# Kernel tuning notes

Hardware: AMD Instinct MI355X
Metric: run time of the kernel (lower is better)

The kernel has to match this reference:

```python
import jax, jax.numpy as jnp
import numpy as np

LN_EPS = 1e-5


def _gru_scan(xg, w_hh, b_hh, H, reverse):
    # xg: [T, B, 3H] precomputed input-gate activations (W_ih x + b_ih)
    B = xg.shape[1]
    h0 = jnp.zeros((B, H), xg.dtype)

    def step(h, xt):
        hg = h @ w_hh.T + b_hh                      # [B, 3H]
        r = jax.nn.sigmoid(xt[:, :H] + hg[:, :H])
        z = jax.nn.sigmoid(xt[:, H:2 * H] + hg[:, H:2 * H])
        n = jnp.tanh(xt[:, 2 * H:] + r * hg[:, 2 * H:])
        h = (1.0 - z) * n + z * h
        return h, h

    _, ys = jax.lax.scan(step, h0, xg, reverse=reverse)
    return ys                                       # [T, B, H]


def setup_inputs() -> dict:
    key = jax.random.key(0)
    ks = jax.random.split(key, 12)
    B, T, I, H = 32, 1000, 512, 512
    s = 1.0 / np.sqrt(H)
    u = lambda k, shape: jax.random.uniform(k, shape, jnp.float32, -s, s)
    return {
        "x": jax.random.normal(ks[0], (B, T, I), jnp.float32),
        "ln_gamma": jnp.ones((I,), jnp.float32),
        "ln_beta": jnp.zeros((I,), jnp.float32),
        "w_ih_f": u(ks[1], (3 * H, I)),
        "w_hh_f": u(ks[2], (3 * H, H)),
        "b_ih_f": u(ks[3], (3 * H,)),
        "b_hh_f": u(ks[4], (3 * H,)),
        "w_ih_b": u(ks[5], (3 * H, I)),
        "w_hh_b": u(ks[6], (3 * H, H)),
        "b_ih_b": u(ks[7], (3 * H,)),
        "b_hh_b": u(ks[8], (3 * H,)),
    }


def reference(x, ln_gamma, ln_beta, w_ih_f, w_hh_f, b_ih_f, b_hh_f,
              w_ih_b, w_hh_b, b_ih_b, b_hh_b):
    H = w_hh_f.shape[1]
    # LayerNorm over last dim
    mu = jnp.mean(x, axis=-1, keepdims=True)
    var = jnp.var(x, axis=-1, keepdims=True)
    xn = (x - mu) * jax.lax.rsqrt(var + LN_EPS) * ln_gamma + ln_beta
    # ReLU6
    xn = jnp.clip(xn, 0.0, 6.0)
    # batch_first -> time-major [T, B, I]
    xt = jnp.transpose(xn, (1, 0, 2))
    # Precompute input projections for both directions
    xg_f = xt @ w_ih_f.T + b_ih_f                   # [T, B, 3H]
    xg_b = xt @ w_ih_b.T + b_ih_b
    yf = _gru_scan(xg_f, w_hh_f, b_hh_f, H, reverse=False)
    yb = _gru_scan(xg_b, w_hh_b, b_hh_b, H, reverse=True)
    y = jnp.concatenate([yf, yb], axis=-1)          # [T, B, 2H]
    # dropout treated as identity (deterministic reference)
    return jnp.transpose(y, (1, 0, 2))              # [B, T, 2H]
```

## Files before the change

kernel.cpp:

```cpp
#include <hip/hip_runtime.h>


typedef _Float16 half8   __attribute__((ext_vector_type(8)));
typedef _Float16 half2_  __attribute__((ext_vector_type(2)));
typedef float    floatx4 __attribute__((ext_vector_type(4)));
typedef float    floatx2 __attribute__((ext_vector_type(2)));
typedef unsigned int uintx4 __attribute__((ext_vector_type(4)));

#define T_LEN 1000
#define NB    32
#define DIM   512

#define XN_OFF   0
#define HB_OFF   32768000
#define CTR_OFF  32899072
#define WS_NEED  32899328

__device__ __forceinline__ float bf2f(unsigned short b) {
  unsigned int u = ((unsigned int)b) << 16; float f; __builtin_memcpy(&f, &u, 4); return f;
}
__device__ __forceinline__ unsigned short f2bf(float f) {
  unsigned int u; __builtin_memcpy(&u, &f, 4);
  u = (u + 0x7FFFu + ((u >> 16) & 1u)) >> 16;
  return (unsigned short)u;
}

__global__ void init_kernel(unsigned int* ws32) {
  const int base = HB_OFF / 4;
  const int n    = (WS_NEED - HB_OFF) / 4;
  for (int i = blockIdx.x * blockDim.x + threadIdx.x; i < n; i += gridDim.x * blockDim.x)
    ws32[base + i] = 0u;
}

__global__ __launch_bounds__(256) void ln_kernel(const void* __restrict__ xin,
                                                 const void* __restrict__ gam,
                                                 const void* __restrict__ bet,
                                                 unsigned short* __restrict__ xn) {
  const bool bf = (((const unsigned int*)gam)[0] != 0x3F800000u);
  const int w = threadIdx.x >> 6, l = threadIdx.x & 63;
  const int row = blockIdx.x * 4 + w;
  const int b = row / T_LEN, t = row - b * T_LEN;

  float v[8], g[8], be[8];
  if (bf) {
    const unsigned int* xp = (const unsigned int*)xin + (row * 512 + l * 8) / 2;
    uintx4 r4 = *(const uintx4*)xp;
    uintx4 g4 = *(const uintx4*)((const unsigned int*)gam + l * 4);
    uintx4 b4 = *(const uintx4*)((const unsigned int*)bet + l * 4);
#pragma unroll
    for (int j = 0; j < 4; ++j) {
      v[2*j]   = bf2f((unsigned short)(r4[j] & 0xFFFFu));
      v[2*j+1] = bf2f((unsigned short)(r4[j] >> 16));
      g[2*j]   = bf2f((unsigned short)(g4[j] & 0xFFFFu));
      g[2*j+1] = bf2f((unsigned short)(g4[j] >> 16));
      be[2*j]  = bf2f((unsigned short)(b4[j] & 0xFFFFu));
      be[2*j+1] = bf2f((unsigned short)(b4[j] >> 16));
    }
  } else {
    const float* xp = (const float*)xin + (size_t)row * 512 + l * 8;
    floatx4 a0 = *(const floatx4*)xp;
    floatx4 a1 = *(const floatx4*)(xp + 4);
    const float* gp = (const float*)gam + l * 8;
    const float* bp = (const float*)bet + l * 8;
#pragma unroll
    for (int j = 0; j < 4; ++j) {
      v[j] = a0[j]; v[4+j] = a1[j];
      g[j] = gp[j]; g[4+j] = gp[4+j];
      be[j] = bp[j]; be[4+j] = bp[4+j];
    }
  }

  float s1 = 0.f, s2 = 0.f;
#pragma unroll
  for (int j = 0; j < 8; ++j) { s1 += v[j]; s2 += v[j] * v[j]; }
#pragma unroll
  for (int m = 1; m < 64; m <<= 1) { s1 += __shfl_xor(s1, m); s2 += __shfl_xor(s2, m); }
  const float mean = s1 * (1.f / 512.f);
  const float var  = s2 * (1.f / 512.f) - mean * mean;
  const float rstd = rsqrtf(var + 1e-5f);

  unsigned int out[4];
#pragma unroll
  for (int j = 0; j < 4; ++j) {
    float f0 = (v[2*j]   - mean) * rstd * g[2*j]   + be[2*j];
    float f1 = (v[2*j+1] - mean) * rstd * g[2*j+1] + be[2*j+1];
    f0 = fminf(fmaxf(f0, 0.f), 6.f);
    f1 = fminf(fmaxf(f1, 0.f), 6.f);
    half2_ hp = { (_Float16)f0, (_Float16)f1 };
    __builtin_memcpy(&out[j], &hp, 4);
  }
  *(uintx4*)(xn + ((size_t)(t * 32 + b) * 512 + l * 8)) = *(uintx4*)out;
}

#define SMEM_BYTES 125312

__global__ __launch_bounds__(256, 1) void gru_kernel(
    const void* __restrict__ wihF, const void* __restrict__ whhF,
    const void* __restrict__ bihF, const void* __restrict__ bhhF,
    const void* __restrict__ wihB, const void* __restrict__ whhB,
    const void* __restrict__ bihB, const void* __restrict__ bhhB,
    const void* __restrict__ gam,
    const unsigned short* __restrict__ xn,
    unsigned short* __restrict__ hb,
    unsigned int* __restrict__ ctr,
    void* __restrict__ yout) {
  extern __shared__ char smem[];
  _Float16* wih = (_Float16*)smem;
  _Float16* whh = (_Float16*)(smem + 49152);
  float* part = (float*)(smem + 98304);
  float* hown = (float*)(smem + 122880);
  float* bihs = (float*)(smem + 124928);
  float* bhhs = (float*)(smem + 125120);

  const bool bf = (((const unsigned int*)gam)[0] != 0x3F800000u);
  const int tid = threadIdx.x;
  const int w = tid >> 6, l = tid & 63, quad = l >> 4, lan = l & 15;
  const int dir = blockIdx.x >> 5, wg = blockIdx.x & 31, c0 = wg * 16;

  const void* Wg[2] = { dir ? wihB : wihF, dir ? whhB : whhF };
  const void* Bg[2] = { dir ? bihB : bihF, dir ? bhhB : bhhF };

  for (int idx = tid; idx < 6144; idx += 256) {
    const int mat = idx / 3072;
    const int r = idx - mat * 3072;
    const int nt = r >> 10, s = (r >> 6) & 15, ln = r & 63;
    const int row = nt * 512 + c0 + (ln & 15);
    const int k0 = s * 32 + (ln >> 4) * 8;
    float tmp[8];
    if (bf) {
      const unsigned int* p = (const unsigned int*)Wg[mat] + (row * 512 + k0) / 2;
      uintx4 r4 = *(const uintx4*)p;
#pragma unroll
      for (int j = 0; j < 4; ++j) {
        tmp[2*j]   = bf2f((unsigned short)(r4[j] & 0xFFFFu));
        tmp[2*j+1] = bf2f((unsigned short)(r4[j] >> 16));
      }
    } else {
      const float* p = (const float*)Wg[mat] + (size_t)row * 512 + k0;
      floatx4 a0 = *(const floatx4*)p;
      floatx4 a1 = *(const floatx4*)(p + 4);
#pragma unroll
      for (int j = 0; j < 4; ++j) { tmp[j] = a0[j]; tmp[4+j] = a1[j]; }
    }
    _Float16* dst = (mat ? whh : wih) + ((size_t)((nt * 16 + s) * 64 + ln)) * 8;
#pragma unroll
    for (int j = 0; j < 8; ++j) dst[j] = (_Float16)tmp[j];
  }
  if (tid < 96) {
    const int mat = tid / 48, i = tid % 48, g_ = i >> 4, c = i & 15;
    const int gi = g_ * 512 + c0 + c;
    float v = bf ? bf2f(((const unsigned short*)Bg[mat])[gi]) : ((const float*)Bg[mat])[gi];
    (mat ? bhhs : bihs)[i] = v;
  }
  for (int i = tid; i < 512; i += 256) hown[i] = 0.f;
  __syncthreads();

  unsigned int* myctr = ctr + dir * 16;
  const int kh = w & 1;
  unsigned short* hb_d = hb + dir * 2 * 16384;
  const _Float16* wb = (w < 2) ? wih : whh;

  for (int t = 0; t < T_LEN; ++t) {
    const int tt = dir ? (T_LEN - 1 - t) : t;
    const int cur = t & 1, nxt = cur ^ 1;

    floatx4 acc[2][3];
#pragma unroll
    for (int mt = 0; mt < 2; ++mt)
#pragma unroll
      for (int nt = 0; nt < 3; ++nt) acc[mt][nt] = (floatx4){0.f, 0.f, 0.f, 0.f};

    if (w < 2) {
      const _Float16* A = (const _Float16*)xn + (size_t)tt * 16384;
      half8 av[2][8];
#pragma unroll
      for (int si = 0; si < 8; ++si) {
        const int s = kh * 8 + si, k0 = s * 32 + quad * 8;
        av[0][si] = *(const half8*)(A + (lan * 512 + k0));
        av[1][si] = *(const half8*)(A + ((16 + lan) * 512 + k0));
      }
#pragma unroll
      for (int si = 0; si < 8; ++si) {
        const int s = kh * 8 + si;
#pragma unroll
        for (int nt = 0; nt < 3; ++nt) {
          half8 bfr = *(const half8*)(wb + ((size_t)((nt * 16 + s) * 64 + l)) * 8);
          acc[0][nt] = __builtin_amdgcn_mfma_f32_16x16x32_f16(av[0][si], bfr, acc[0][nt], 0, 0, 0);
          acc[1][nt] = __builtin_amdgcn_mfma_f32_16x16x32_f16(av[1][si], bfr, acc[1][nt], 0, 0, 0);
        }
      }
    } else {
      const unsigned long long* A = (const unsigned long long*)(hb_d + cur * 16384);
      union HU { unsigned long long q[2]; half8 h; };
      HU u[2][8];
#pragma unroll
      for (int si = 0; si < 8; ++si) {
        const int s = kh * 8 + si, k0 = s * 32 + quad * 8;
        const unsigned long long* p0 = A + (lan * 512 + k0) / 4;
        const unsigned long long* p1 = A + ((16 + lan) * 512 + k0) / 4;
        u[0][si].q[0] = __hip_atomic_load(p0,     __ATOMIC_RELAXED, __HIP_MEMORY_SCOPE_AGENT);
        u[0][si].q[1] = __hip_atomic_load(p0 + 1, __ATOMIC_RELAXED, __HIP_MEMORY_SCOPE_AGENT);
        u[1][si].q[0] = __hip_atomic_load(p1,     __ATOMIC_RELAXED, __HIP_MEMORY_SCOPE_AGENT);
        u[1][si].q[1] = __hip_atomic_load(p1 + 1, __ATOMIC_RELAXED, __HIP_MEMORY_SCOPE_AGENT);
      }
#pragma unroll
      for (int si = 0; si < 8; ++si) {
        const int s = kh * 8 + si;
#pragma unroll
        for (int nt = 0; nt < 3; ++nt) {
          half8 bfr = *(const half8*)(wb + ((size_t)((nt * 16 + s) * 64 + l)) * 8);
          acc[0][nt] = __builtin_amdgcn_mfma_f32_16x16x32_f16(u[0][si].h, bfr, acc[0][nt], 0, 0, 0);
          acc[1][nt] = __builtin_amdgcn_mfma_f32_16x16x32_f16(u[1][si].h, bfr, acc[1][nt], 0, 0, 0);
        }
      }
    }

#pragma unroll
    for (int mt = 0; mt < 2; ++mt)
#pragma unroll
      for (int nt = 0; nt < 3; ++nt) {
        float* p = part + ((w * 6 + mt * 3 + nt) << 8);
#pragma unroll
        for (int r = 0; r < 4; ++r) p[(quad * 4 + r) * 16 + lan] = acc[mt][nt][r];
      }
    __syncthreads();

    {
      const int b = tid >> 3, cp = tid & 7;
      const int mt = b >> 4, mr = b & 15;
      float hv[2];
#pragma unroll
      for (int e = 0; e < 2; ++e) {
        const int c = cp * 2 + e;
        const int o = mr * 16 + c;
#define PT(W_, NT_) part[(((W_) * 6 + mt * 3 + (NT_)) << 8) + o]
        const float xr = PT(0, 0) + PT(1, 0) + bihs[c];
        const float xz = PT(0, 1) + PT(1, 1) + bihs[16 + c];
        const float xg = PT(0, 2) + PT(1, 2) + bihs[32 + c];
        const float hr = PT(2, 0) + PT(3, 0) + bhhs[c];
        const float hz = PT(2, 1) + PT(3, 1) + bhhs[16 + c];
        const float hg = PT(2, 2) + PT(3, 2) + bhhs[32 + c];
#undef PT
        const float rr = 1.f / (1.f + __expf(-(xr + hr)));
        const float zz = 1.f / (1.f + __expf(-(xz + hz)));
        float a = xg + rr * hg;
        a = fminf(fmaxf(a, -15.f), 15.f);
        const float e2 = __expf(2.f * a);
        const float nn = (e2 - 1.f) / (e2 + 1.f);
        const float hp = hown[b * 16 + c];
        const float hvv = (1.f - zz) * nn + zz * hp;
        hown[b * 16 + c] = hvv;
        hv[e] = hvv;
      }
      half2_ pk = { (_Float16)hv[0], (_Float16)hv[1] };
      unsigned int pu; __builtin_memcpy(&pu, &pk, 4);
      unsigned int* hdst = (unsigned int*)(hb_d + nxt * 16384 + b * 512 + c0 + cp * 2);
      __hip_atomic_store(hdst, pu, __ATOMIC_RELAXED, __HIP_MEMORY_SCOPE_AGENT);
      const size_t yo = ((size_t)b * T_LEN + tt) * 1024 + dir * 512 + c0 + cp * 2;
      if (bf) {
        unsigned int yp = (unsigned int)f2bf(hv[0]) | ((unsigned int)f2bf(hv[1]) << 16);
        *(unsigned int*)((unsigned short*)yout + yo) = yp;
      } else {
        *(floatx2*)((float*)yout + yo) = (floatx2){hv[0], hv[1]};
      }
    }

    if (t < T_LEN - 1) {
      __syncthreads();
      if (tid == 0) {
        __hip_atomic_fetch_add(myctr, 1u, __ATOMIC_RELAXED, __HIP_MEMORY_SCOPE_AGENT);
        const unsigned int tgt = 32u * (unsigned int)(t + 1);
        while (__hip_atomic_load(myctr, __ATOMIC_RELAXED, __HIP_MEMORY_SCOPE_AGENT) < tgt)
          __builtin_amdgcn_s_sleep(1);
      }
      __syncthreads();
    }
  }
}

extern "C" void kernel_launch(void* const* d_in, const int* in_sizes, int n_in,
                              void* d_out, int out_size, void* d_ws, size_t ws_size,
                              hipStream_t stream) {
  if (ws_size < (size_t)WS_NEED) return;

  (void)hipFuncSetAttribute((const void*)gru_kernel,
                            hipFuncAttributeMaxDynamicSharedMemorySize, 131072);

  const void* x   = d_in[0];
  const void* gam = d_in[1];
  const void* bet = d_in[2];
  const void* wihF = d_in[3]; const void* whhF = d_in[4];
  const void* bihF = d_in[5]; const void* bhhF = d_in[6];
  const void* wihB = d_in[7]; const void* whhB = d_in[8];
  const void* bihB = d_in[9]; const void* bhhB = d_in[10];

  unsigned short* xnp = (unsigned short*)((char*)d_ws + XN_OFF);
  unsigned short* hbp = (unsigned short*)((char*)d_ws + HB_OFF);
  unsigned int*   cp  = (unsigned int*)((char*)d_ws + CTR_OFF);

  init_kernel<<<64, 256, 0, stream>>>((unsigned int*)d_ws);
  ln_kernel<<<8000, 256, 0, stream>>>(x, gam, bet, xnp);
  gru_kernel<<<64, 256, SMEM_BYTES, stream>>>(wihF, whhF, bihF, bhhF,
                                              wihB, whhB, bihB, bhhB,
                                              gam, xnp, hbp, cp, d_out);
}
```

Measured before the change: 5.283 ms.

## Overlap next-step input projection with grid barrier wait using per-block flags

Takes the input-projection MFMA for step t+1 off the recurrent critical path. Each block now computes it, together with the prefetch of the following x slice, while it waits for the other blocks to publish h. All four waves now split the K dimension of both matmuls and accumulate into double-buffered LDS partials with atomicAdd. The single shared atomic counter is replaced by per-block flags, polled by 32 threads. This shortens each serial step, at the cost of LDS atomics, extra zeroing passes and more registers.

```diff
diff --git a/kernel.cpp b/kernel.cpp
--- a/kernel.cpp
+++ b/kernel.cpp
@@ -8,13 +8,19 @@
 typedef unsigned int uintx4 __attribute__((ext_vector_type(4)));
 
 #define T_LEN 1000
-#define NB    32
-#define DIM   512
 
 #define XN_OFF   0
 #define HB_OFF   32768000
 #define CTR_OFF  32899072
-#define WS_NEED  32899328
+#define WS_NEED  32903168
+
+#define L_WIH    0
+#define L_WHH    49152
+#define L_PART   98304
+#define L_HOWN   116736
+#define L_BIH    118784
+#define L_BHH    118976
+#define SMEM_BYTES 119168
 
 __device__ __forceinline__ float bf2f(unsigned short b) {
   unsigned int u = ((unsigned int)b) << 16; float f; __builtin_memcpy(&f, &u, 4); return f;
@@ -92,8 +98,6 @@
   *(uintx4*)(xn + ((size_t)(t * 32 + b) * 512 + l * 8)) = *(uintx4*)out;
 }
 
-#define SMEM_BYTES 125312
-
 __global__ __launch_bounds__(256, 1) void gru_kernel(
     const void* __restrict__ wihF, const void* __restrict__ whhF,
     const void* __restrict__ bihF, const void* __restrict__ bhhF,
@@ -102,20 +106,21 @@
     const void* __restrict__ gam,
     const unsigned short* __restrict__ xn,
     unsigned short* __restrict__ hb,
-    unsigned int* __restrict__ ctr,
+    unsigned int* __restrict__ flags,
     void* __restrict__ yout) {
   extern __shared__ char smem[];
-  _Float16* wih = (_Float16*)smem;
-  _Float16* whh = (_Float16*)(smem + 49152);
-  float* part = (float*)(smem + 98304);
-  float* hown = (float*)(smem + 122880);
-  float* bihs = (float*)(smem + 124928);
-  float* bhhs = (float*)(smem + 125120);
-
+  _Float16* wihL = (_Float16*)(smem + L_WIH);
+  _Float16* whhL = (_Float16*)(smem + L_WHH);
+  float* part = (float*)(smem + L_PART);
+  float* hown = (float*)(smem + L_HOWN);
+  float* bihs = (float*)(smem + L_BIH);
+  float* bhhs = (float*)(smem + L_BHH);
+
+  const int tid = threadIdx.x;
+  const int dir = blockIdx.x >> 5, wg = blockIdx.x & 31, c0 = wg * 16;
   const bool bf = (((const unsigned int*)gam)[0] != 0x3F800000u);
-  const int tid = threadIdx.x;
   const int w = tid >> 6, l = tid & 63, quad = l >> 4, lan = l & 15;
-  const int dir = blockIdx.x >> 5, wg = blockIdx.x & 31, c0 = wg * 16;
+  const int w4 = w * 4;
 
   const void* Wg[2] = { dir ? wihB : wihF, dir ? whhB : whhF };
   const void* Bg[2] = { dir ? bihB : bihF, dir ? bhhB : bhhF };
@@ -142,7 +147,7 @@
 #pragma unroll
       for (int j = 0; j < 4; ++j) { tmp[j] = a0[j]; tmp[4+j] = a1[j]; }
     }
-    _Float16* dst = (mat ? whh : wih) + ((size_t)((nt * 16 + s) * 64 + ln)) * 8;
+    _Float16* dst = (mat ? whhL : wihL) + ((size_t)((nt * 16 + s) * 64 + ln)) * 8;
 #pragma unroll
     for (int j = 0; j < 8; ++j) dst[j] = (_Float16)tmp[j];
   }
@@ -153,97 +158,119 @@
     (mat ? bhhs : bihs)[i] = v;
   }
   for (int i = tid; i < 512; i += 256) hown[i] = 0.f;
+  for (int i = tid; i < 4608; i += 256) part[i] = 0.f;
   __syncthreads();
 
-  unsigned int* myctr = ctr + dir * 16;
-  const int kh = w & 1;
+  unsigned int* myflag = flags + dir * 512 + wg * 16;
+  unsigned int* pollfl = flags + dir * 512 + tid * 16;
   unsigned short* hb_d = hb + dir * 2 * 16384;
-  const _Float16* wb = (w < 2) ? wih : whh;
+
+  union HU { uintx4 u; half8 h; unsigned long long q[2]; };
+  HU av[8];
+
+  auto av_fill = [&](int ttx) {
+    const _Float16* A = (const _Float16*)xn + (size_t)ttx * 16384;
+#pragma unroll
+    for (int i = 0; i < 8; ++i) {
+      const int mt = i >> 2, si = i & 3;
+      const int k0 = (w4 + si) * 32 + quad * 8;
+      av[i].h = *(const half8*)(A + ((mt * 16 + lan) * 512 + k0));
+    }
+  };
+
+  auto xg_compute = [&](int pb) {
+    floatx4 xa[2][3];
+#pragma unroll
+    for (int mt = 0; mt < 2; ++mt)
+#pragma unroll
+      for (int nt = 0; nt < 3; ++nt) xa[mt][nt] = (floatx4){0.f, 0.f, 0.f, 0.f};
+#pragma unroll
+    for (int si = 0; si < 4; ++si) {
+      const int s = w4 + si;
+#pragma unroll
+      for (int nt = 0; nt < 3; ++nt) {
+        half8 bfr = *(const half8*)(wihL + ((size_t)((nt * 16 + s) * 64 + l)) * 8);
+        xa[0][nt] = __builtin_amdgcn_mfma_f32_16x16x32_f16(av[si].h,     bfr, xa[0][nt], 0, 0, 0);
+        xa[1][nt] = __builtin_amdgcn_mfma_f32_16x16x32_f16(av[4 + si].h, bfr, xa[1][nt], 0, 0, 0);
+      }
+    }
+#pragma unroll
+    for (int mt = 0; mt < 2; ++mt)
+#pragma unroll
+      for (int nt = 0; nt < 3; ++nt) {
+        const int g = (nt == 2) ? 3 : nt;
+        float* p = part + (pb * 8 + mt * 4 + g) * 288;
+#pragma unroll
+        for (int r = 0; r < 4; ++r)
+          atomicAdd(&p[(quad * 4 + r) * 18 + lan], xa[mt][nt][r]);
+      }
+  };
+
+  av_fill(dir ? (T_LEN - 1) : 0);
+  xg_compute(0);
+  av_fill(dir ? (T_LEN - 2) : 1);
 
   for (int t = 0; t < T_LEN; ++t) {
     const int tt = dir ? (T_LEN - 1 - t) : t;
     const int cur = t & 1, nxt = cur ^ 1;
 
-    floatx4 acc[2][3];
-#pragma unroll
-    for (int mt = 0; mt < 2; ++mt)
-#pragma unroll
-      for (int nt = 0; nt < 3; ++nt) acc[mt][nt] = (floatx4){0.f, 0.f, 0.f, 0.f};
-
-    if (w < 2) {
-      const _Float16* A = (const _Float16*)xn + (size_t)tt * 16384;
-      half8 av[2][8];
-#pragma unroll
-      for (int si = 0; si < 8; ++si) {
-        const int s = kh * 8 + si, k0 = s * 32 + quad * 8;
-        av[0][si] = *(const half8*)(A + (lan * 512 + k0));
-        av[1][si] = *(const half8*)(A + ((16 + lan) * 512 + k0));
-      }
-#pragma unroll
-      for (int si = 0; si < 8; ++si) {
-        const int s = kh * 8 + si;
+    {
+      floatx4 acc[2][3];
+#pragma unroll
+      for (int mt = 0; mt < 2; ++mt)
+#pragma unroll
+        for (int nt = 0; nt < 3; ++nt) acc[mt][nt] = (floatx4){0.f, 0.f, 0.f, 0.f};
+
+      const unsigned short* hbase = hb_d + cur * 16384;
+      HU ha[8];
+#pragma unroll
+      for (int i = 0; i < 8; ++i) {
+        const int mt = i >> 2, si = i & 3;
+        const int k0 = (w4 + si) * 32 + quad * 8;
+        unsigned long long* p =
+            (unsigned long long*)(hbase + (mt * 16 + lan) * 512 + k0);
+        ha[i].q[0] = __hip_atomic_load(p,     __ATOMIC_RELAXED, __HIP_MEMORY_SCOPE_AGENT);
+        ha[i].q[1] = __hip_atomic_load(p + 1, __ATOMIC_RELAXED, __HIP_MEMORY_SCOPE_AGENT);
+      }
+#pragma unroll
+      for (int si = 0; si < 4; ++si) {
+        const int s = w4 + si;
 #pragma unroll
         for (int nt = 0; nt < 3; ++nt) {
-          half8 bfr = *(const half8*)(wb + ((size_t)((nt * 16 + s) * 64 + l)) * 8);
-          acc[0][nt] = __builtin_amdgcn_mfma_f32_16x16x32_f16(av[0][si], bfr, acc[0][nt], 0, 0, 0);
-          acc[1][nt] = __builtin_amdgcn_mfma_f32_16x16x32_f16(av[1][si], bfr, acc[1][nt], 0, 0, 0);
+          half8 bfr = *(const half8*)(whhL + ((size_t)((nt * 16 + s) * 64 + l)) * 8);
+          acc[0][nt] = __builtin_amdgcn_mfma_f32_16x16x32_f16(ha[si].h,     bfr, acc[0][nt], 0, 0, 0);
+          acc[1][nt] = __builtin_amdgcn_mfma_f32_16x16x32_f16(ha[4 + si].h, bfr, acc[1][nt], 0, 0, 0);
         }
       }
-    } else {
-      const unsigned long long* A = (const unsigned long long*)(hb_d + cur * 16384);
-      union HU { unsigned long long q[2]; half8 h; };
-      HU u[2][8];
-#pragma unroll
-      for (int si = 0; si < 8; ++si) {
-        const int s = kh * 8 + si, k0 = s * 32 + quad * 8;
-        const unsigned long long* p0 = A + (lan * 512 + k0) / 4;
-        const unsigned long long* p1 = A + ((16 + lan) * 512 + k0) / 4;
-        u[0][si].q[0] = __hip_atomic_load(p0,     __ATOMIC_RELAXED, __HIP_MEMORY_SCOPE_AGENT);
-        u[0][si].q[1] = __hip_atomic_load(p0 + 1, __ATOMIC_RELAXED, __HIP_MEMORY_SCOPE_AGENT);
-        u[1][si].q[0] = __hip_atomic_load(p1,     __ATOMIC_RELAXED, __HIP_MEMORY_SCOPE_AGENT);
-        u[1][si].q[1] = __hip_atomic_load(p1 + 1, __ATOMIC_RELAXED, __HIP_MEMORY_SCOPE_AGENT);
-      }
-#pragma unroll
-      for (int si = 0; si < 8; ++si) {
-        const int s = kh * 8 + si;
+#pragma unroll
+      for (int mt = 0; mt < 2; ++mt)
 #pragma unroll
         for (int nt = 0; nt < 3; ++nt) {
-          half8 bfr = *(const half8*)(wb + ((size_t)((nt * 16 + s) * 64 + l)) * 8);
-          acc[0][nt] = __builtin_amdgcn_mfma_f32_16x16x32_f16(u[0][si].h, bfr, acc[0][nt], 0, 0, 0);
-          acc[1][nt] = __builtin_amdgcn_mfma_f32_16x16x32_f16(u[1][si].h, bfr, acc[1][nt], 0, 0, 0);
+          float* p = part + (cur * 8 + mt * 4 + nt) * 288;
+#pragma unroll
+          for (int r = 0; r < 4; ++r)
+            atomicAdd(&p[(quad * 4 + r) * 18 + lan], acc[mt][nt][r]);
         }
-      }
-    }
-
-#pragma unroll
-    for (int mt = 0; mt < 2; ++mt)
-#pragma unroll
-      for (int nt = 0; nt < 3; ++nt) {
-        float* p = part + ((w * 6 + mt * 3 + nt) << 8);
-#pragma unroll
-        for (int r = 0; r < 4; ++r) p[(quad * 4 + r) * 16 + lan] = acc[mt][nt][r];
-      }
+    }
     __syncthreads();
 
+    float hv0, hv1;
+    const int b = tid >> 3, cp = tid & 7;
     {
-      const int b = tid >> 3, cp = tid & 7;
       const int mt = b >> 4, mr = b & 15;
+      const float* pb = part + (cur * 8 + mt * 4) * 288;
       float hv[2];
 #pragma unroll
       for (int e = 0; e < 2; ++e) {
         const int c = cp * 2 + e;
-        const int o = mr * 16 + c;
-#define PT(W_, NT_) part[(((W_) * 6 + mt * 3 + (NT_)) << 8) + o]
-        const float xr = PT(0, 0) + PT(1, 0) + bihs[c];
-        const float xz = PT(0, 1) + PT(1, 1) + bihs[16 + c];
-        const float xg = PT(0, 2) + PT(1, 2) + bihs[32 + c];
-        const float hr = PT(2, 0) + PT(3, 0) + bhhs[c];
-        const float hz = PT(2, 1) + PT(3, 1) + bhhs[16 + c];
-        const float hg = PT(2, 2) + PT(3, 2) + bhhs[32 + c];
-#undef PT
-        const float rr = 1.f / (1.f + __expf(-(xr + hr)));
-        const float zz = 1.f / (1.f + __expf(-(xz + hz)));
-        float a = xg + rr * hg;
+        const int o = mr * 18 + c;
+        const float sr = pb[o]       + bihs[c]      + bhhs[c];
+        const float sz = pb[288 + o] + bihs[16 + c] + bhhs[16 + c];
+        const float hn = pb[576 + o] + bhhs[32 + c];
+        const float xg = pb[864 + o] + bihs[32 + c];
+        const float rr = 1.f / (1.f + __expf(-sr));
+        const float zz = 1.f / (1.f + __expf(-sz));
+        float a = xg + rr * hn;
         a = fminf(fmaxf(a, -15.f), 15.f);
         const float e2 = __expf(2.f * a);
         const float nn = (e2 - 1.f) / (e2 + 1.f);
@@ -252,28 +279,49 @@
         hown[b * 16 + c] = hvv;
         hv[e] = hvv;
       }
-      half2_ pk = { (_Float16)hv[0], (_Float16)hv[1] };
+      hv0 = hv[0]; hv1 = hv[1];
+      half2_ pk = { (_Float16)hv0, (_Float16)hv1 };
       unsigned int pu; __builtin_memcpy(&pu, &pk, 4);
       unsigned int* hdst = (unsigned int*)(hb_d + nxt * 16384 + b * 512 + c0 + cp * 2);
       __hip_atomic_store(hdst, pu, __ATOMIC_RELAXED, __HIP_MEMORY_SCOPE_AGENT);
-      const size_t yo = ((size_t)b * T_LEN + tt) * 1024 + dir * 512 + c0 + cp * 2;
+    }
+    {
+      float* zb = part + nxt * 8 * 288;
+      for (int i = tid; i < 2304; i += 256) zb[i] = 0.f;
+    }
+
+    const size_t yo = ((size_t)b * T_LEN + tt) * 1024 + dir * 512 + c0 + cp * 2;
+
+    if (t < T_LEN - 1) {
+      __syncthreads();
+      if (tid == 0)
+        __hip_atomic_store(myflag, (unsigned int)(t + 1), __ATOMIC_RELAXED,
+                           __HIP_MEMORY_SCOPE_AGENT);
       if (bf) {
-        unsigned int yp = (unsigned int)f2bf(hv[0]) | ((unsigned int)f2bf(hv[1]) << 16);
+        unsigned int yp = (unsigned int)f2bf(hv0) | ((unsigned int)f2bf(hv1) << 16);
         *(unsigned int*)((unsigned short*)yout + yo) = yp;
       } else {
-        *(floatx2*)((float*)yout + yo) = (floatx2){hv[0], hv[1]};
-      }
-    }
-
-    if (t < T_LEN - 1) {
+        *(floatx2*)((float*)yout + yo) = (floatx2){hv0, hv1};
+      }
+      xg_compute(nxt);
+      {
+        int tn = dir ? (T_LEN - 3 - t) : (t + 2);
+        tn = tn < 0 ? 0 : (tn >= T_LEN ? T_LEN - 1 : tn);
+        av_fill(tn);
+      }
+      if (tid < 32) {
+        const unsigned int tgt = (unsigned int)(t + 1);
+        while (__hip_atomic_load(pollfl, __ATOMIC_RELAXED, __HIP_MEMORY_SCOPE_AGENT) < tgt)
+          __builtin_amdgcn_s_sleep(1);
+      }
       __syncthreads();
-      if (tid == 0) {
-        __hip_atomic_fetch_add(myctr, 1u, __ATOMIC_RELAXED, __HIP_MEMORY_SCOPE_AGENT);
-        const unsigned int tgt = 32u * (unsigned int)(t + 1);
-        while (__hip_atomic_load(myctr, __ATOMIC_RELAXED, __HIP_MEMORY_SCOPE_AGENT) < tgt)
-          __builtin_amdgcn_s_sleep(1);
-      }
-      __syncthreads();
+    } else {
+      if (bf) {
+        unsigned int yp = (unsigned int)f2bf(hv0) | ((unsigned int)f2bf(hv1) << 16);
+        *(unsigned int*)((unsigned short*)yout + yo) = yp;
+      } else {
+        *(floatx2*)((float*)yout + yo) = (floatx2){hv0, hv1};
+      }
     }
   }
 }
@@ -296,11 +344,11 @@
 
   unsigned short* xnp = (unsigned short*)((char*)d_ws + XN_OFF);
   unsigned short* hbp = (unsigned short*)((char*)d_ws + HB_OFF);
-  unsigned int*   cp  = (unsigned int*)((char*)d_ws + CTR_OFF);
+  unsigned int*   fp  = (unsigned int*)((char*)d_ws + CTR_OFF);
 
   init_kernel<<<64, 256, 0, stream>>>((unsigned int*)d_ws);
   ln_kernel<<<8000, 256, 0, stream>>>(x, gam, bet, xnp);
   gru_kernel<<<64, 256, SMEM_BYTES, stream>>>(wihF, whhF, bihF, bhhF,
                                               wihB, whhB, bihB, bhhB,
-                                              gam, xnp, hbp, cp, d_out);
-}
+                                              gam, xnp, hbp, fp, d_out);
+}
```

Result: slower. 18.54 ms (+250.8%).
